# Kernel optimization log

Measured on AMD Instinct MI355X. Metric: run time of the kernel, lower is better.

Reference implementation:

```python
import jax, jax.numpy as jnp
import numpy as np

D = 768  # in_channels == out_channels (forced by residual + shared LayerNorm)
B, S = 8, 2048


def setup_inputs() -> dict:
    key = jax.random.key(0)
    ks = jax.random.split(key, 5)
    x = jax.random.normal(ks[0], (B, S, D), dtype=jnp.float32)
    # LayerNorm params
    ln_g = jnp.ones((D,), dtype=jnp.float32)
    ln_b = jnp.zeros((D,), dtype=jnp.float32)
    # Q/K linear params (torch Linear: y = x @ W.T + b)
    scale = 1.0 / np.sqrt(D)
    Wq = jax.random.uniform(ks[1], (D, D), jnp.float32, -scale, scale)
    bq = jax.random.uniform(ks[2], (D,), jnp.float32, -scale, scale)
    Wk = jax.random.uniform(ks[3], (D, D), jnp.float32, -scale, scale)
    bk = jax.random.uniform(ks[4], (D,), jnp.float32, -scale, scale)
    return {"x": x, "ln_g": ln_g, "ln_b": ln_b, "Wq": Wq, "bq": bq, "Wk": Wk, "bk": bk}


def _layernorm(x, g, b, eps=1e-5):
    mu = jnp.mean(x, axis=-1, keepdims=True)
    var = jnp.mean(jnp.square(x - mu), axis=-1, keepdims=True)
    return (x - mu) * jax.lax.rsqrt(var + eps) * g + b


def reference(x, ln_g, ln_b, Wq, bq, Wk, bk):
    origin = x
    xn = _layernorm(x, ln_g, ln_b)
    Q = xn @ Wq.T + bq  # [B,S,D]
    K = xn @ Wk.T + bk  # [B,S,D]
    scores = jnp.einsum('bsd,btd->bst', Q, K) / jnp.sqrt(jnp.asarray(D, x.dtype))
    attn = jax.nn.softmax(scores, axis=-1)  # [B,S,S]
    out = jnp.einsum('bst,btd->bsd', attn, origin) + origin
    # note: original then computes relu(layernorm(out)) but returns `out` (dead code)
    return out
```

## Files before the change

### kernel.cpp

```cpp
#include <hip/hip_runtime.h>

typedef __bf16 bf16;
typedef __bf16 v8bf __attribute__((ext_vector_type(8)));
typedef __bf16 v4bf __attribute__((ext_vector_type(4)));
typedef float  v4f  __attribute__((ext_vector_type(4)));

__device__ __forceinline__ void gload_lds16(const void* g, void* l) {
    __builtin_amdgcn_global_load_lds(
        (const __attribute__((address_space(1))) void*)g,
        (__attribute__((address_space(3))) void*)l, 16, 0, 0);
}

__global__ __launch_bounds__(256)
void ln_cast(const float* __restrict__ x, const float* __restrict__ g,
             const float* __restrict__ b, bf16* __restrict__ xn,
             bf16* __restrict__ xv, float* __restrict__ L)
{
    const long row = blockIdx.x;
    const float* xr = x + row * 768;
    const int tid = threadIdx.x;
    const int wave = tid >> 6, lane = tid & 63;

    if (row < 64) L[row * 256 + tid] = 0.0f;

    float a0 = xr[tid], a1 = xr[tid + 256], a2 = xr[tid + 512];
    float s = a0 + a1 + a2;
    #pragma unroll
    for (int off = 32; off; off >>= 1) s += __shfl_xor(s, off);
    __shared__ float sh[4], sh2[4];
    if (!lane) sh[wave] = s;
    __syncthreads();
    const float mu = (sh[0] + sh[1] + sh[2] + sh[3]) * (1.0f / 768.0f);

    float d0 = a0 - mu, d1 = a1 - mu, d2 = a2 - mu;
    float ss = d0 * d0 + d1 * d1 + d2 * d2;
    #pragma unroll
    for (int off = 32; off; off >>= 1) ss += __shfl_xor(ss, off);
    if (!lane) sh2[wave] = ss;
    __syncthreads();
    const float var = (sh2[0] + sh2[1] + sh2[2] + sh2[3]) * (1.0f / 768.0f);
    const float rstd = rsqrtf(var + 1e-5f);

    bf16* xnr = xn + row * 768;
    bf16* xvr = xv + row * 768;
    xnr[tid]       = (bf16)(d0 * rstd * g[tid]       + b[tid]);
    xnr[tid + 256] = (bf16)(d1 * rstd * g[tid + 256] + b[tid + 256]);
    xnr[tid + 512] = (bf16)(d2 * rstd * g[tid + 512] + b[tid + 512]);
    xvr[tid]       = (bf16)a0;
    xvr[tid + 256] = (bf16)a1;
    xvr[tid + 512] = (bf16)a2;
}

__global__ __launch_bounds__(256)
void cvt_w(const float* __restrict__ Wq, const float* __restrict__ Wk,
           bf16* __restrict__ Wcat)
{
    const int z = blockIdx.y;
    const float* src = z ? Wk : Wq;
    bf16* dst = Wcat + (long)z * 768 * 768;
    const int i = (blockIdx.x * 256 + threadIdx.x) * 4;
    const float4 v = *(const float4*)(src + i);
    v4bf o = {(bf16)v.x, (bf16)v.y, (bf16)v.z, (bf16)v.w};
    *(v4bf*)(dst + i) = o;
}

__global__ __launch_bounds__(256)
void transpose_bf(const bf16* __restrict__ in, bf16* __restrict__ outT)
{
    __shared__ __attribute__((aligned(16))) bf16 tile[64 * 64];
    const int t0 = blockIdx.x * 64, d0 = blockIdx.y * 64;
    in   += (long)blockIdx.z * 2048 * 768;
    outT += (long)blockIdx.z * 768 * 2048;
    const int tid = threadIdx.x;

    #pragma unroll
    for (int it = 0; it < 2; ++it) {
        const int lin = it * 256 + tid;
        const int r = lin >> 3;
        const int g = lin & 7;
        const int pg = g ^ (r & 7) ^ ((r >> 3) & 7);
        v8bf v = *(const v8bf*)(in + (long)(t0 + r) * 768 + d0 + g * 8);
        *(v8bf*)(tile + r * 64 + pg * 8) = v;
    }
    __syncthreads();
    #pragma unroll
    for (int it = 0; it < 2; ++it) {
        const int lin = it * 256 + tid;
        const int dd = lin >> 3;
        const int tb = lin & 7;
        v8bf o;
        #pragma unroll
        for (int j = 0; j < 8; ++j) {
            const int t = tb * 8 + j;
            const int pg = (dd >> 3) ^ (t & 7) ^ ((t >> 3) & 7);
            o[j] = tile[t * 64 + pg * 8 + (dd & 7)];
        }
        *(v8bf*)(outT + (long)(d0 + dd) * 2048 + t0 + tb * 8) = o;
    }
}

__global__ __launch_bounds__(256)
void gemm_qk(const bf16* __restrict__ A, const bf16* __restrict__ W,
             const float* __restrict__ bq, const float* __restrict__ bk,
             float qscale, bf16* __restrict__ Qb, bf16* __restrict__ Kb)
{
    __shared__ __attribute__((aligned(16))) bf16 As[2][128 * 32];
    __shared__ __attribute__((aligned(16))) bf16 Bs[2][128 * 32];

    const int bx = blockIdx.x;
    const int r = bx & 7, j = bx >> 3;
    const int m0 = (r * 16 + j / 12) * 128;
    const int n0 = (j % 12) * 128;

    const int tid = threadIdx.x, wave = tid >> 6, lane = tid & 63;
    const bf16* Ab = A + (long)m0 * 768;
    const bf16* Bb = W + (long)n0 * 768;

    const int lrow = lane >> 2;
    const int lk   = (lane & 3) * 8;
    const int wm = (wave >> 1) * 64, wn = (wave & 1) * 64;
    const int lr = lane & 15, lq = lane >> 4;

    v4f acc[4][4] = {};

    for (int kk = 0; kk < 768; kk += 64) {
        #pragma unroll
        for (int p = 0; p < 2; ++p)
            #pragma unroll
            for (int it = 0; it < 2; ++it) {
                const int c = it * 4 + wave;
                const int row = c * 16 + lrow;
                gload_lds16(Ab + (long)row * 768 + kk + p * 32 + lk,
                            (char*)As[p] + c * 1024);
                gload_lds16(Bb + (long)row * 768 + kk + p * 32 + lk,
                            (char*)Bs[p] + c * 1024);
            }
        __syncthreads();

        #pragma unroll
        for (int p = 0; p < 2; ++p) {
            v8bf af[4], bfr[4];
            #pragma unroll
            for (int i = 0; i < 4; ++i)
                af[i] = *(const v8bf*)(As[p] + (wm + i * 16 + lr) * 32 + lq * 8);
            #pragma unroll
            for (int jj = 0; jj < 4; ++jj)
                bfr[jj] = *(const v8bf*)(Bs[p] + (wn + jj * 16 + lr) * 32 + lq * 8);
            #pragma unroll
            for (int i = 0; i < 4; ++i)
                #pragma unroll
                for (int jj = 0; jj < 4; ++jj)
                    acc[i][jj] = __builtin_amdgcn_mfma_f32_16x16x32_bf16(
                        af[i], bfr[jj], acc[i][jj], 0, 0, 0);
        }
        __syncthreads();
    }

    const bool isQ = (n0 < 768);
    const float* bias = isQ ? bq : bk;
    const float sc = isQ ? qscale : 1.0f;
    bf16* C = isQ ? Qb : Kb;
    const int c0 = isQ ? n0 : n0 - 768;

    #pragma unroll
    for (int i = 0; i < 4; ++i) {
        #pragma unroll
        for (int rr = 0; rr < 4; ++rr) {
            const int row = m0 + wm + i * 16 + lq * 4 + rr;
            #pragma unroll
            for (int jj = 0; jj < 4; ++jj) {
                const int col = c0 + wn + jj * 16 + lr;
                C[(long)row * 768 + col] = (bf16)((acc[i][jj][rr] + bias[col]) * sc);
            }
        }
    }
}

__global__ __launch_bounds__(512, 2)
void gemm_scores(const bf16* __restrict__ Q, const bf16* __restrict__ K,
                 bf16* __restrict__ E, float* __restrict__ L)
{
    __shared__ __attribute__((aligned(16))) bf16 lds[3][24576];

    const int bx = blockIdx.x;
    const int batch = bx & 7, j = bx >> 3;
    const int mt = j >> 3, nt = j & 7;
    const int m0 = mt * 128, n0 = nt * 256;

    const bf16* Ag = Q + (long)batch * 2048 * 768 + (long)m0 * 768;
    const bf16* Bg = K + (long)batch * 2048 * 768 + (long)n0 * 768;
    bf16* C = E + (long)batch * 2048 * 2048;
    float* Lb = L + (long)batch * 2048;

    const int tid = threadIdx.x, wv = tid >> 6, lane = tid & 63;
    const int wr = wv >> 2, wc = wv & 3;
    const int lr = lane & 15, lq = lane >> 4;

    auto stageA = [&](int slot, int kk, int a) {
        const int lin = a * 64 + lane;
        const int r = lin >> 3;
        const int ck = (lin & 7) ^ (r & 7);
        gload_lds16(Ag + (long)r * 768 + kk + ck * 8,
                    (char*)lds[slot] + a * 1024);
    };
    auto stageB = [&](int slot, int kk, int b) {
        const int lin = b * 64 + lane;
        const int r = lin >> 3;
        const int ck = (lin & 7) ^ (r & 7);
        gload_lds16(Bg + (long)r * 768 + kk + ck * 8,
                    (char*)lds[slot] + 16384 + b * 1024);
    };

    v4f acc[4][4] = {};
    const int NT = 12;

    #pragma unroll
    for (int tt = 0; tt < 2; ++tt) {
        stageA(tt, tt * 64, wv * 2 + 0);
        stageA(tt, tt * 64, wv * 2 + 1);
        #pragma unroll
        for (int l = 0; l < 4; ++l) stageB(tt, tt * 64, wv * 4 + l);
    }
    asm volatile("s_waitcnt vmcnt(6)" ::: "memory");
    __builtin_amdgcn_s_barrier();

    for (int t = 0; t < NT; ++t) {
        const int cur = t % 3;
        const int nxt = (t + 2) % 3;
        const int kk2 = (t + 2) * 64;
        const bf16* As = lds[cur];
        const bf16* Bs = lds[cur] + 8192;
        const bool pre = (t + 2 < NT);

        v8bf af[4][2], bfr[2][2];
        #pragma unroll
        for (int i = 0; i < 4; ++i) {
            const int row = wr * 64 + i * 16 + lr;
            #pragma unroll
            for (int s = 0; s < 2; ++s)
                af[i][s] = *(const v8bf*)(As + row * 64 +
                                          (((s * 4 + lq) ^ (row & 7)) << 3));
        }
        #pragma unroll
        for (int jn = 0; jn < 2; ++jn) {
            const int row = wc * 64 + jn * 16 + lr;
            #pragma unroll
            for (int s = 0; s < 2; ++s)
                bfr[jn][s] = *(const v8bf*)(Bs + row * 64 +
                                            (((s * 4 + lq) ^ (row & 7)) << 3));
        }
        if (pre) {
            stageA(nxt, kk2, wv * 2 + 0);
            stageA(nxt, kk2, wv * 2 + 1);
            stageB(nxt, kk2, wv * 4 + 0);
        }
        __builtin_amdgcn_s_barrier();
        asm volatile("s_waitcnt lgkmcnt(0)" ::: "memory");
        __builtin_amdgcn_s_setprio(1);
        #pragma unroll
        for (int s = 0; s < 2; ++s)
            #pragma unroll
            for (int i = 0; i < 4; ++i)
                #pragma unroll
                for (int jn = 0; jn < 2; ++jn)
                    acc[i][jn] = __builtin_amdgcn_mfma_f32_16x16x32_bf16(
                        af[i][s], bfr[jn][s], acc[i][jn], 0, 0, 0);
        __builtin_amdgcn_s_setprio(0);
        __builtin_amdgcn_s_barrier();

        #pragma unroll
        for (int jn = 0; jn < 2; ++jn) {
            const int row = wc * 64 + (jn + 2) * 16 + lr;
            #pragma unroll
            for (int s = 0; s < 2; ++s)
                bfr[jn][s] = *(const v8bf*)(Bs + row * 64 +
                                            (((s * 4 + lq) ^ (row & 7)) << 3));
        }
        if (pre) {
            stageB(nxt, kk2, wv * 4 + 1);
            stageB(nxt, kk2, wv * 4 + 2);
            stageB(nxt, kk2, wv * 4 + 3);
        }
        __builtin_amdgcn_s_barrier();
        asm volatile("s_waitcnt lgkmcnt(0)" ::: "memory");
        __builtin_amdgcn_s_setprio(1);
        #pragma unroll
        for (int s = 0; s < 2; ++s)
            #pragma unroll
            for (int i = 0; i < 4; ++i)
                #pragma unroll
                for (int jn = 0; jn < 2; ++jn)
                    acc[i][jn + 2] = __builtin_amdgcn_mfma_f32_16x16x32_bf16(
                        af[i][s], bfr[jn][s], acc[i][jn + 2], 0, 0, 0);
        __builtin_amdgcn_s_setprio(0);
        if (t < NT - 2)       asm volatile("s_waitcnt vmcnt(6)" ::: "memory");
        else if (t == NT - 2) asm volatile("s_waitcnt vmcnt(0)" ::: "memory");
        __builtin_amdgcn_s_barrier();
    }

    #pragma unroll
    for (int i = 0; i < 4; ++i) {
        #pragma unroll
        for (int rr = 0; rr < 4; ++rr) {
            const int row = m0 + wr * 64 + i * 16 + lq * 4 + rr;
            float e[4], rs = 0.f;
            #pragma unroll
            for (int jn = 0; jn < 4; ++jn) {
                e[jn] = __expf(acc[i][jn][rr]);
                rs += e[jn];
            }
            #pragma unroll
            for (int off = 1; off < 16; off <<= 1) rs += __shfl_xor(rs, off);
            if (lr == 0) atomicAdd(&Lb[row], rs);
            #pragma unroll
            for (int jn = 0; jn < 4; ++jn) {
                const int col = n0 + wc * 64 + jn * 16 + lr;
                C[(long)row * 2048 + col] = (bf16)e[jn];
            }
        }
    }
}

__global__ __launch_bounds__(256)
void gemm_pv(const bf16* __restrict__ P, const bf16* __restrict__ VT,
             const float* __restrict__ L, const float* __restrict__ Xres,
             float* __restrict__ Out)
{
    __shared__ __attribute__((aligned(16))) bf16 As[2][64 * 32];
    __shared__ __attribute__((aligned(16))) bf16 Bs[2][128 * 32];

    const int bx = blockIdx.x;
    const int batch = bx & 7, j = bx >> 3;
    const int m0 = (j / 6) * 64;
    const int n0 = (j % 6) * 128;

    const bf16* Ab = P  + (long)batch * 2048 * 2048 + (long)m0 * 2048;
    const bf16* Bb = VT + (long)batch * 768 * 2048  + (long)n0 * 2048;
    const float* Lb = L + (long)batch * 2048;
    const float* Xr = Xres + (long)batch * 2048 * 768;
    float* O = Out + (long)batch * 2048 * 768;

    const int tid = threadIdx.x, wave = tid >> 6, lane = tid & 63;
    const int lrow = lane >> 2;
    const int lk   = (lane & 3) * 8;
    const int wm = (wave >> 1) * 32, wn = (wave & 1) * 64;
    const int lr = lane & 15, lq = lane >> 4;

    v4f acc[2][4] = {};

    for (int kk = 0; kk < 2048; kk += 64) {
        #pragma unroll
        for (int p = 0; p < 2; ++p) {
            gload_lds16(Ab + (long)(wave * 16 + lrow) * 2048 + kk + p * 32 + lk,
                        (char*)As[p] + wave * 1024);
            #pragma unroll
            for (int it = 0; it < 2; ++it) {
                const int c = it * 4 + wave;
                gload_lds16(Bb + (long)(c * 16 + lrow) * 2048 + kk + p * 32 + lk,
                            (char*)Bs[p] + c * 1024);
            }
        }
        __syncthreads();

        #pragma unroll
        for (int p = 0; p < 2; ++p) {
            v8bf af[2], bfr[4];
            #pragma unroll
            for (int i = 0; i < 2; ++i)
                af[i] = *(const v8bf*)(As[p] + (wm + i * 16 + lr) * 32 + lq * 8);
            #pragma unroll
            for (int jj = 0; jj < 4; ++jj)
                bfr[jj] = *(const v8bf*)(Bs[p] + (wn + jj * 16 + lr) * 32 + lq * 8);
            #pragma unroll
            for (int i = 0; i < 2; ++i)
                #pragma unroll
                for (int jj = 0; jj < 4; ++jj)
                    acc[i][jj] = __builtin_amdgcn_mfma_f32_16x16x32_bf16(
                        af[i], bfr[jj], acc[i][jj], 0, 0, 0);
        }
        __syncthreads();
    }

    #pragma unroll
    for (int i = 0; i < 2; ++i) {
        #pragma unroll
        for (int rr = 0; rr < 4; ++rr) {
            const int row = m0 + wm + i * 16 + lq * 4 + rr;
            const float invL = 1.0f / Lb[row];
            #pragma unroll
            for (int jj = 0; jj < 4; ++jj) {
                const int col = n0 + wn + jj * 16 + lr;
                const long idx = (long)row * 768 + col;
                O[idx] = acc[i][jj][rr] * invL + Xr[idx];
            }
        }
    }
}

extern "C" void kernel_launch(void* const* d_in, const int* in_sizes, int n_in,
                              void* d_out, int out_size, void* d_ws, size_t ws_size,
                              hipStream_t stream)
{
    const float* x    = (const float*)d_in[0];
    const float* ln_g = (const float*)d_in[1];
    const float* ln_b = (const float*)d_in[2];
    const float* Wq   = (const float*)d_in[3];
    const float* bq   = (const float*)d_in[4];
    const float* Wk   = (const float*)d_in[5];
    const float* bk   = (const float*)d_in[6];
    float* out = (float*)d_out;

    const long R = 8L * 2048;
    char* ws = (char*)d_ws;
    size_t off = 0;
    auto take = [&](size_t bytes) -> char* {
        char* p = ws + off;
        off += (bytes + 255) & ~(size_t)255;
        return p;
    };
    bf16*  xn   = (bf16*)take(R * 768 * 2);
    bf16*  xv   = (bf16*)take(R * 768 * 2);
    bf16*  Qb   = (bf16*)take(R * 768 * 2);
    bf16*  Kb   = (bf16*)take(R * 768 * 2);
    bf16*  Wcat = (bf16*)take(1536L * 768 * 2);
    float* Lrow = (float*)take(R * 4);
    bf16*  Sc   = (bf16*)take(8L * 2048 * 2048 * 2);

    ln_cast<<<R, 256, 0, stream>>>(x, ln_g, ln_b, xn, xv, Lrow);
    cvt_w<<<dim3(576, 2), 256, 0, stream>>>(Wq, Wk, Wcat);

    const float qscale = 0.036084391824351615f;
    gemm_qk<<<1536, 256, 0, stream>>>(xn, Wcat, bq, bk, qscale, Qb, Kb);

    bf16* xvT = xn;
    transpose_bf<<<dim3(32, 12, 8), 256, 0, stream>>>(xv, xvT);

    gemm_scores<<<1024, 512, 0, stream>>>(Qb, Kb, Sc, Lrow);
    gemm_pv<<<1536, 256, 0, stream>>>(Sc, xvT, Lrow, x, out);
}
```

Before: 341.4 us.

## Rewrite PV GEMM with 128x384 tiles, swizzled LDS, and interleaved prefetch

The P·V GEMM now uses 512-thread blocks computing 128x384 output tiles (256 blocks instead of 1536) with a 64-wide K step. The LDS layout is XOR-swizzled, and the loads for the next K tile are split across two compute phases with double buffering and raised wave priority around the MFMA work. The intent is to cut redundant global reads of P and V, avoid LDS bank conflicts, and overlap loads with matrix math. The larger per-wave accumulators raise register pressure, and 256 blocks may not fill all CUs evenly.

```diff
diff --git a/kernel.cpp b/kernel.cpp
--- a/kernel.cpp
+++ b/kernel.cpp
@@ -321,77 +321,138 @@
     }
 }
 
-__global__ __launch_bounds__(256)
+__global__ __launch_bounds__(512, 2)
 void gemm_pv(const bf16* __restrict__ P, const bf16* __restrict__ VT,
              const float* __restrict__ L, const float* __restrict__ Xres,
              float* __restrict__ Out)
 {
-    __shared__ __attribute__((aligned(16))) bf16 As[2][64 * 32];
-    __shared__ __attribute__((aligned(16))) bf16 Bs[2][128 * 32];
+    __shared__ __attribute__((aligned(16))) bf16 lds[2][32768];
 
     const int bx = blockIdx.x;
     const int batch = bx & 7, j = bx >> 3;
-    const int m0 = (j / 6) * 64;
-    const int n0 = (j % 6) * 128;
-
-    const bf16* Ab = P  + (long)batch * 2048 * 2048 + (long)m0 * 2048;
-    const bf16* Bb = VT + (long)batch * 768 * 2048  + (long)n0 * 2048;
+    const int m0 = (j >> 1) * 128;
+    const int n0 = (j & 1) * 384;
+
+    const bf16* Ag = P  + (long)batch * 2048 * 2048 + (long)m0 * 2048;
+    const bf16* Bg = VT + (long)batch * 768 * 2048  + (long)n0 * 2048;
     const float* Lb = L + (long)batch * 2048;
     const float* Xr = Xres + (long)batch * 2048 * 768;
     float* O = Out + (long)batch * 2048 * 768;
 
-    const int tid = threadIdx.x, wave = tid >> 6, lane = tid & 63;
-    const int lrow = lane >> 2;
-    const int lk   = (lane & 3) * 8;
-    const int wm = (wave >> 1) * 32, wn = (wave & 1) * 64;
+    const int tid = threadIdx.x, wv = tid >> 6, lane = tid & 63;
+    const int wr = wv >> 2, wc = wv & 3;
     const int lr = lane & 15, lq = lane >> 4;
 
-    v4f acc[2][4] = {};
-
-    for (int kk = 0; kk < 2048; kk += 64) {
-        #pragma unroll
-        for (int p = 0; p < 2; ++p) {
-            gload_lds16(Ab + (long)(wave * 16 + lrow) * 2048 + kk + p * 32 + lk,
-                        (char*)As[p] + wave * 1024);
-            #pragma unroll
-            for (int it = 0; it < 2; ++it) {
-                const int c = it * 4 + wave;
-                gload_lds16(Bb + (long)(c * 16 + lrow) * 2048 + kk + p * 32 + lk,
-                            (char*)Bs[p] + c * 1024);
-            }
-        }
-        __syncthreads();
-
-        #pragma unroll
-        for (int p = 0; p < 2; ++p) {
-            v8bf af[2], bfr[4];
-            #pragma unroll
-            for (int i = 0; i < 2; ++i)
-                af[i] = *(const v8bf*)(As[p] + (wm + i * 16 + lr) * 32 + lq * 8);
-            #pragma unroll
-            for (int jj = 0; jj < 4; ++jj)
-                bfr[jj] = *(const v8bf*)(Bs[p] + (wn + jj * 16 + lr) * 32 + lq * 8);
-            #pragma unroll
-            for (int i = 0; i < 2; ++i)
+    auto stageA = [&](int slot, int kk, int a) {
+        const int lin = a * 64 + lane;
+        const int r = lin >> 3;
+        const int ck = (lin & 7) ^ (r & 7);
+        gload_lds16(Ag + (long)r * 2048 + kk + ck * 8,
+                    (char*)lds[slot] + a * 1024);
+    };
+    auto stageB = [&](int slot, int kk, int b) {
+        const int lin = b * 64 + lane;
+        const int r = lin >> 3;
+        const int ck = (lin & 7) ^ (r & 7);
+        gload_lds16(Bg + (long)r * 2048 + kk + ck * 8,
+                    (char*)lds[slot] + 16384 + b * 1024);
+    };
+
+    v4f acc[4][6] = {};
+    const int NT = 32;
+
+    stageA(0, 0, wv * 2 + 0);
+    stageA(0, 0, wv * 2 + 1);
+    #pragma unroll
+    for (int l = 0; l < 6; ++l) stageB(0, 0, wv * 6 + l);
+    asm volatile("s_waitcnt vmcnt(0)" ::: "memory");
+    __builtin_amdgcn_s_barrier();
+
+    for (int t = 0; t < NT; ++t) {
+        const int cur = t & 1, nxt = cur ^ 1;
+        const int kk1 = (t + 1) * 64;
+        const bf16* As = lds[cur];
+        const bf16* Bs = lds[cur] + 8192;
+        const bool pre = (t + 1 < NT);
+
+        v8bf af[4][2], bfr[3][2];
+        #pragma unroll
+        for (int i = 0; i < 4; ++i) {
+            const int row = wr * 64 + i * 16 + lr;
+            #pragma unroll
+            for (int s = 0; s < 2; ++s)
+                af[i][s] = *(const v8bf*)(As + row * 64 +
+                                          (((s * 4 + lq) ^ (row & 7)) << 3));
+        }
+        #pragma unroll
+        for (int jn = 0; jn < 3; ++jn) {
+            const int row = wc * 96 + jn * 16 + lr;
+            #pragma unroll
+            for (int s = 0; s < 2; ++s)
+                bfr[jn][s] = *(const v8bf*)(Bs + row * 64 +
+                                            (((s * 4 + lq) ^ (row & 7)) << 3));
+        }
+        if (pre) {
+            stageA(nxt, kk1, wv * 2 + 0);
+            stageA(nxt, kk1, wv * 2 + 1);
+            stageB(nxt, kk1, wv * 6 + 0);
+            stageB(nxt, kk1, wv * 6 + 1);
+        }
+        __builtin_amdgcn_s_barrier();
+        asm volatile("s_waitcnt lgkmcnt(0)" ::: "memory");
+        __builtin_amdgcn_s_setprio(1);
+        #pragma unroll
+        for (int s = 0; s < 2; ++s)
+            #pragma unroll
+            for (int i = 0; i < 4; ++i)
                 #pragma unroll
-                for (int jj = 0; jj < 4; ++jj)
-                    acc[i][jj] = __builtin_amdgcn_mfma_f32_16x16x32_bf16(
-                        af[i], bfr[jj], acc[i][jj], 0, 0, 0);
-        }
-        __syncthreads();
-    }
-
-    #pragma unroll
-    for (int i = 0; i < 2; ++i) {
+                for (int jn = 0; jn < 3; ++jn)
+                    acc[i][jn] = __builtin_amdgcn_mfma_f32_16x16x32_bf16(
+                        af[i][s], bfr[jn][s], acc[i][jn], 0, 0, 0);
+        __builtin_amdgcn_s_setprio(0);
+        __builtin_amdgcn_s_barrier();
+
+        #pragma unroll
+        for (int jn = 0; jn < 3; ++jn) {
+            const int row = wc * 96 + (jn + 3) * 16 + lr;
+            #pragma unroll
+            for (int s = 0; s < 2; ++s)
+                bfr[jn][s] = *(const v8bf*)(Bs + row * 64 +
+                                            (((s * 4 + lq) ^ (row & 7)) << 3));
+        }
+        if (pre) {
+            stageB(nxt, kk1, wv * 6 + 2);
+            stageB(nxt, kk1, wv * 6 + 3);
+            stageB(nxt, kk1, wv * 6 + 4);
+            stageB(nxt, kk1, wv * 6 + 5);
+        }
+        __builtin_amdgcn_s_barrier();
+        asm volatile("s_waitcnt lgkmcnt(0)" ::: "memory");
+        __builtin_amdgcn_s_setprio(1);
+        #pragma unroll
+        for (int s = 0; s < 2; ++s)
+            #pragma unroll
+            for (int i = 0; i < 4; ++i)
+                #pragma unroll
+                for (int jn = 0; jn < 3; ++jn)
+                    acc[i][jn + 3] = __builtin_amdgcn_mfma_f32_16x16x32_bf16(
+                        af[i][s], bfr[jn][s], acc[i][jn + 3], 0, 0, 0);
+        __builtin_amdgcn_s_setprio(0);
+        if (pre) asm volatile("s_waitcnt vmcnt(0)" ::: "memory");
+        __builtin_amdgcn_s_barrier();
+    }
+
+    #pragma unroll
+    for (int i = 0; i < 4; ++i) {
         #pragma unroll
         for (int rr = 0; rr < 4; ++rr) {
-            const int row = m0 + wm + i * 16 + lq * 4 + rr;
+            const int row = m0 + wr * 64 + i * 16 + lq * 4 + rr;
             const float invL = 1.0f / Lb[row];
             #pragma unroll
-            for (int jj = 0; jj < 4; ++jj) {
-                const int col = n0 + wn + jj * 16 + lr;
+            for (int jn = 0; jn < 6; ++jn) {
+                const int col = n0 + wc * 96 + jn * 16 + lr;
                 const long idx = (long)row * 768 + col;
-                O[idx] = acc[i][jj][rr] * invL + Xr[idx];
+                O[idx] = acc[i][jn][rr] * invL + Xr[idx];
             }
         }
     }
@@ -436,5 +497,5 @@
     transpose_bf<<<dim3(32, 12, 8), 256, 0, stream>>>(xv, xvT);
 
     gemm_scores<<<1024, 512, 0, stream>>>(Qb, Kb, Sc, Lrow);
-    gemm_pv<<<1536, 256, 0, stream>>>(Sc, xvT, Lrow, x, out);
-}
+    gemm_pv<<<256, 512, 0, stream>>>(Sc, xvT, Lrow, x, out);
+}
```

Measured after the change: 335.7 us. No clear change (-1.7%).
